# Performance work log

Measured on AMD Instinct MI355X. Metric: run time of the kernel, lower is better.

The kernel has to match this reference:

```python
import jax, jax.numpy as jnp
import numpy as np
import math

B, S, D, H, W = 4, 8192, 1024, 16, 512  # batch, seq, d_model, heads, attention_window
HD = D // H


def setup_inputs() -> dict:
    key = jax.random.key(0)
    ks = jax.random.split(key, 5)
    scale = 0.02
    return {
        "x": jax.random.normal(ks[0], (B, S, D), dtype=jnp.float32),
        "wq": jax.random.normal(ks[1], (D, D), dtype=jnp.float32) * scale,
        "bq": jnp.zeros((D,), dtype=jnp.float32),
        "wk": jax.random.normal(ks[2], (D, D), dtype=jnp.float32) * scale,
        "bk": jnp.zeros((D,), dtype=jnp.float32),
        "wv": jax.random.normal(ks[3], (D, D), dtype=jnp.float32) * scale,
        "bv": jnp.zeros((D,), dtype=jnp.float32),
        "wo": jax.random.normal(ks[4], (D, D), dtype=jnp.float32) * scale,
        "bo": jnp.zeros((D,), dtype=jnp.float32),
    }


def reference(x, wq, bq, wk, bk, wv, bv, wo, bo):
    # torch Linear: y = x @ W.T + b
    q = (x @ wq.T + bq).reshape(B, S, H, HD)
    k = (x @ wk.T + bk).reshape(B, S, H, HD)
    v = (x @ wv.T + bv).reshape(B, S, H, HD)

    nb = S // W  # number of query blocks
    qb = q.reshape(B, nb, W, H, HD)

    # pad keys/values by W at the front so every block sees a 2W key window
    kp = jnp.pad(k, ((0, 0), (W, 0), (0, 0), (0, 0)))
    vp = jnp.pad(v, ((0, 0), (W, 0), (0, 0), (0, 0)))
    # padded key indices for block n: [n*W, n*W + 2W) <-> original [n*W - W, n*W + W)
    idx = jnp.arange(nb)[:, None] * W + jnp.arange(2 * W)[None, :]  # [nb, 2W]
    kb = kp[:, idx]  # [B, nb, 2W, H, HD]
    vb = vp[:, idx]  # [B, nb, 2W, H, HD]

    scores = jnp.einsum('bnqhd,bnkhd->bnhqk', qb, kb) / math.sqrt(HD)
    valid = (idx >= W)  # padded (out-of-range) keys only occur for block 0
    scores = jnp.where(valid[None, :, None, None, :], scores, -jnp.inf)
    attn = jax.nn.softmax(scores, axis=-1)  # softmax over the block's key window

    out = jnp.einsum('bnhqk,bnkhd->bnqhd', attn, vb).reshape(B, S, D)
    return out @ wo.T + bo
```

## Files before the change

### kernel.cpp

```cpp
#include <hip/hip_runtime.h>
#include <hip/hip_bf16.h>
#include <cstdint>

typedef __bf16 bf16;
typedef __attribute__((ext_vector_type(8))) __bf16 bf16x8;
typedef __attribute__((ext_vector_type(4))) __bf16 bf16x4;
typedef __attribute__((ext_vector_type(4))) float f32x4;
typedef __attribute__((ext_vector_type(16))) float f32x16;
typedef __attribute__((ext_vector_type(4))) unsigned int u32x4;

#define B_ 4
#define S_ 8192
#define D_ 1024
#define H_ 16
#define HD_ 64
#define W_ 512
#define M_ (B_*S_)

#define EXP2F(x) __builtin_amdgcn_exp2f(x)
#define MFMA16(a,b,c) __builtin_amdgcn_mfma_f32_16x16x32_bf16(a,b,c,0,0,0)
#define MFMA32(a,b,c) __builtin_amdgcn_mfma_f32_32x32x16_bf16(a,b,c,0,0,0)

__device__ __forceinline__ void async16(const void* g, void* l) {
  __builtin_amdgcn_global_load_lds(
      (const __attribute__((address_space(1))) unsigned int*)g,
      (__attribute__((address_space(3))) unsigned int*)l, 16, 0, 0);
}

__global__ void cast_f32_bf16(const float* __restrict__ in, bf16* __restrict__ out, int n4) {
  int i = blockIdx.x * blockDim.x + threadIdx.x;
  int stride = gridDim.x * blockDim.x;
  for (; i < n4; i += stride) {
    f32x4 v = ((const f32x4*)in)[i];
    bf16x4 o = { (bf16)v[0], (bf16)v[1], (bf16)v[2], (bf16)v[3] };
    ((bf16x4*)out)[i] = o;
  }
}

template<int MODE>
__global__ void __launch_bounds__(256, 2) gemm_bt(
    const bf16* __restrict__ A, const bf16* __restrict__ Bw,
    const float* __restrict__ bias, void* __restrict__ outp, float scale)
{
  constexpr int K = D_, N = D_;
  __shared__ bf16 As[2][128*32];
  __shared__ bf16 Bs[2][128*32];
  int bid = blockIdx.x;
  int nid = (bid & 7) * 256 + (bid >> 3);
  int bm = nid >> 3, bn = nid & 7;
  const int tid = threadIdx.x, lane = tid & 63;
  const int w = tid >> 6, wr = w >> 1, wc = w & 1;
  f32x4 acc[4][4] = {};
  const int r0 = tid >> 2;
  const int kbyte = (tid & 3) * 16;
  const char* Ab = (const char*)(A + (size_t)bm * 128 * K);
  const char* Bb = (const char*)(Bw + (size_t)bn * 128 * K);

  auto stage = [&](int kt, int buf) {
    const size_t cb = (size_t)kt * 2 + kbyte;
    async16(Ab + (size_t)r0      * (K*2) + cb, (char*)&As[buf][0] + tid*16);
    async16(Ab + (size_t)(r0+64) * (K*2) + cb, (char*)&As[buf][0] + 4096 + tid*16);
    async16(Bb + (size_t)r0      * (K*2) + cb, (char*)&Bs[buf][0] + tid*16);
    async16(Bb + (size_t)(r0+64) * (K*2) + cb, (char*)&Bs[buf][0] + 4096 + tid*16);
  };

  stage(0, 0);
  for (int i = 0; i < 32; ++i) {
    int cur = i & 1;
    if (i < 31) {
      stage((i + 1) * 32, cur ^ 1);
      asm volatile("s_waitcnt vmcnt(4)" ::: "memory");
    } else {
      asm volatile("s_waitcnt vmcnt(0)" ::: "memory");
    }
    asm volatile("s_barrier" ::: "memory");
    bf16x8 a[4], b[4];
#pragma unroll
    for (int mi = 0; mi < 4; ++mi)
      a[mi] = *(const bf16x8*)(&As[cur][0] + (wr*64 + mi*16 + (lane & 15))*32 + ((lane >> 4)*8));
#pragma unroll
    for (int ni = 0; ni < 4; ++ni)
      b[ni] = *(const bf16x8*)(&Bs[cur][0] + (wc*64 + ni*16 + (lane & 15))*32 + ((lane >> 4)*8));
#pragma unroll
    for (int mi = 0; mi < 4; ++mi)
#pragma unroll
      for (int ni = 0; ni < 4; ++ni)
        acc[mi][ni] = MFMA16(a[mi], b[ni], acc[mi][ni]);
    asm volatile("s_barrier" ::: "memory");
  }
  int row0 = bm*128 + wr*64, col0 = bn*128 + wc*64;
  int rsub = (lane >> 4) * 4;
#pragma unroll
  for (int ni = 0; ni < 4; ++ni) {
    int col = col0 + ni*16 + (lane & 15);
    float bz = bias[col];
#pragma unroll
    for (int mi = 0; mi < 4; ++mi) {
#pragma unroll
      for (int r = 0; r < 4; ++r) {
        int row = row0 + mi*16 + rsub + r;
        float v = (acc[mi][ni][r] + bz) * scale;
        if (MODE == 0) {
          ((bf16*)outp)[(size_t)row * N + col] = (bf16)v;
        } else if (MODE == 1) {
          ((bf16*)outp)[((size_t)(row >> 13) * D_ + col) * S_ + (row & (S_-1))] = (bf16)v;
        } else {
          ((float*)outp)[(size_t)row * N + col] = v;
        }
      }
    }
  }
}

__global__ void __launch_bounds__(256, 3) attn_kernel(
    const bf16* __restrict__ Q, const bf16* __restrict__ Kb,
    const bf16* __restrict__ Vt, bf16* __restrict__ Ao)
{
  __shared__ char Klds[2][8192];
  __shared__ char Vlds[2][8192];
  int x = blockIdx.x;
  int qt = (x >> 3) & 3;
  int g  = (x & 7) + 8 * (x >> 5);
  int h = g & 15, n = (g >> 4) & 15, b = g >> 8;
  int tid = threadIdx.x, lane = tid & 63, w = tid >> 6;
  int hi = lane >> 5, qv = lane & 31;
  int qrow = n * W_ + qt * 128 + w * 32;

  const bf16* Qrow = Q + ((size_t)(b * S_ + qrow + qv)) * D_ + h * 64;
  bf16x8 Qf[4];
#pragma unroll
  for (int s = 0; s < 4; ++s) Qf[s] = *(const bf16x8*)(Qrow + s * 16 + hi * 8);

  const bf16* Kg = Kb + ((size_t)b * S_) * D_ + h * 64;
  const bf16* Vg = Vt + ((size_t)(b * H_ + h) * HD_) * S_;

  const int srow = tid >> 3, scol = tid & 7;
  const int sswz = (srow & 7) << 4;
  const int fswq = (qv & 7) << 4;

  f32x16 O0 = {}, O1 = {};
  float m_r = -3.0e38f, l_r = 0.f;

  const int c0 = (n == 0) ? 8 : 0;
  const int ksbase = (n - 1) * W_;

  u32x4 pk0, pk1, pv0, pv1;
  {
    int ks = ksbase + c0 * 64;
    pk0 = *(const u32x4*)(Kg + (size_t)(ks + srow)      * D_ + scol * 8);
    pk1 = *(const u32x4*)(Kg + (size_t)(ks + srow + 32) * D_ + scol * 8);
    pv0 = *(const u32x4*)(Vg + (size_t)srow        * S_ + ks + scol * 8);
    pv1 = *(const u32x4*)(Vg + (size_t)(srow + 32) * S_ + ks + scol * 8);
    *(u32x4*)(Klds[0] + srow        * 128 + ((scol * 16) ^ sswz)) = pk0;
    *(u32x4*)(Klds[0] + (srow + 32) * 128 + ((scol * 16) ^ sswz)) = pk1;
    *(u32x4*)(Vlds[0] + srow        * 128 + ((scol * 16) ^ sswz)) = pv0;
    *(u32x4*)(Vlds[0] + (srow + 32) * 128 + ((scol * 16) ^ sswz)) = pv1;
  }
  __syncthreads();
  int cur = 0;
  for (int c = c0; c < 16; ++c) {
    bool pre = (c < 15);
    if (pre) {
      int ks2 = ksbase + (c + 1) * 64;
      pk0 = *(const u32x4*)(Kg + (size_t)(ks2 + srow)      * D_ + scol * 8);
      pk1 = *(const u32x4*)(Kg + (size_t)(ks2 + srow + 32) * D_ + scol * 8);
      pv0 = *(const u32x4*)(Vg + (size_t)srow        * S_ + ks2 + scol * 8);
      pv1 = *(const u32x4*)(Vg + (size_t)(srow + 32) * S_ + ks2 + scol * 8);
    }
    const char* kbuf = Klds[cur];
    const char* vbuf = Vlds[cur];
    f32x16 C0 = {}, C1 = {};
    __builtin_amdgcn_s_setprio(1);
#pragma unroll
    for (int s = 0; s < 4; ++s) {
      bf16x8 k0 = *(const bf16x8*)(kbuf + qv * 128        + ((s * 32 + hi * 16) ^ fswq));
      bf16x8 k1 = *(const bf16x8*)(kbuf + (32 + qv) * 128 + ((s * 32 + hi * 16) ^ fswq));
      C0 = MFMA32(k0, Qf[s], C0);
      C1 = MFMA32(k1, Qf[s], C1);
    }
    __builtin_amdgcn_s_setprio(0);
    float mx = C0[0];
#pragma unroll
    for (int r = 1; r < 16; ++r) mx = fmaxf(mx, C0[r]);
#pragma unroll
    for (int r = 0; r < 16; ++r) mx = fmaxf(mx, C1[r]);
    mx = fmaxf(mx, __shfl_xor(mx, 32));
    if (!__all(mx - m_r <= 8.0f)) {
      float mn = fmaxf(m_r, mx);
      float sc = EXP2F(m_r - mn);
      m_r = mn;
      l_r *= sc;
#pragma unroll
      for (int r = 0; r < 16; ++r) { O0[r] *= sc; O1[r] *= sc; }
    }
    float ls = 0.f;
    float p0[16], p1[16];
#pragma unroll
    for (int r = 0; r < 16; ++r) {
      p0[r] = EXP2F(C0[r] - m_r);
      p1[r] = EXP2F(C1[r] - m_r);
      ls += p0[r] + p1[r];
    }
    l_r += ls;
    unsigned int L0[8], L1[8];
#pragma unroll
    for (int t = 0; t < 8; ++t) {
      asm("v_cvt_pk_bf16_f32 %0, %1, %2" : "=v"(L0[t]) : "v"(p0[2*t]), "v"(p0[2*t+1]));
      asm("v_cvt_pk_bf16_f32 %0, %1, %2" : "=v"(L1[t]) : "v"(p1[2*t]), "v"(p1[2*t+1]));
    }
    asm volatile("v_permlane32_swap_b32 %0, %1" : "+v"(L0[0]), "+v"(L0[2]));
    asm volatile("v_permlane32_swap_b32 %0, %1" : "+v"(L0[1]), "+v"(L0[3]));
    asm volatile("v_permlane32_swap_b32 %0, %1" : "+v"(L0[4]), "+v"(L0[6]));
    asm volatile("v_permlane32_swap_b32 %0, %1" : "+v"(L0[5]), "+v"(L0[7]));
    asm volatile("v_permlane32_swap_b32 %0, %1" : "+v"(L1[0]), "+v"(L1[2]));
    asm volatile("v_permlane32_swap_b32 %0, %1" : "+v"(L1[1]), "+v"(L1[3]));
    asm volatile("v_permlane32_swap_b32 %0, %1" : "+v"(L1[4]), "+v"(L1[6]));
    asm volatile("v_permlane32_swap_b32 %0, %1" : "+v"(L1[5]), "+v"(L1[7]));
    u32x4 F[2][2];
    F[0][0] = u32x4{L0[0], L0[1], L0[2], L0[3]};
    F[0][1] = u32x4{L0[4], L0[5], L0[6], L0[7]};
    F[1][0] = u32x4{L1[0], L1[1], L1[2], L1[3]};
    F[1][1] = u32x4{L1[4], L1[5], L1[6], L1[7]};
    __builtin_amdgcn_s_setprio(1);
#pragma unroll
    for (int T = 0; T < 2; ++T)
#pragma unroll
      for (int s = 0; s < 2; ++s) {
        bf16x8 pf = *(bf16x8*)&F[T][s];
        int kbyteoff = T * 64 + s * 32 + hi * 16;
        bf16x8 v0 = *(const bf16x8*)(vbuf + qv * 128        + (kbyteoff ^ fswq));
        bf16x8 v1 = *(const bf16x8*)(vbuf + (32 + qv) * 128 + (kbyteoff ^ fswq));
        O0 = MFMA32(v0, pf, O0);
        O1 = MFMA32(v1, pf, O1);
      }
    __builtin_amdgcn_s_setprio(0);
    if (pre) {
      int nb = cur ^ 1;
      *(u32x4*)(Klds[nb] + srow        * 128 + ((scol * 16) ^ sswz)) = pk0;
      *(u32x4*)(Klds[nb] + (srow + 32) * 128 + ((scol * 16) ^ sswz)) = pk1;
      *(u32x4*)(Vlds[nb] + srow        * 128 + ((scol * 16) ^ sswz)) = pv0;
      *(u32x4*)(Vlds[nb] + (srow + 32) * 128 + ((scol * 16) ^ sswz)) = pv1;
    }
    __syncthreads();
    cur ^= 1;
  }
  float lt = l_r + __shfl_xor(l_r, 32);
  float inv = 1.0f / lt;
  size_t obase = ((size_t)(b * S_ + qrow + qv)) * D_ + h * 64;
#pragma unroll
  for (int ot = 0; ot < 2; ++ot) {
#pragma unroll
    for (int rq = 0; rq < 4; ++rq) {
      int hd = ot * 32 + 8 * rq + 4 * hi;
      bf16x4 ov;
#pragma unroll
      for (int j = 0; j < 4; ++j) {
        float val = (ot == 0 ? O0[rq*4 + j] : O1[rq*4 + j]) * inv;
        ov[j] = (bf16)val;
      }
      *(bf16x4*)(Ao + obase + hd) = ov;
    }
  }
}

extern "C" void kernel_launch(void* const* d_in, const int* in_sizes, int n_in,
                              void* d_out, int out_size, void* d_ws, size_t ws_size,
                              hipStream_t stream) {
  const float* x  = (const float*)d_in[0];
  const float* wq = (const float*)d_in[1];
  const float* bq = (const float*)d_in[2];
  const float* wk = (const float*)d_in[3];
  const float* bk = (const float*)d_in[4];
  const float* wv = (const float*)d_in[5];
  const float* bv = (const float*)d_in[6];
  const float* wo = (const float*)d_in[7];
  const float* bo = (const float*)d_in[8];
  float* out = (float*)d_out;

  char* ws = (char*)d_ws;
  const size_t sz = (size_t)M_ * D_ * 2;
  bf16* xb  = (bf16*)(ws + 0*sz);
  bf16* qb  = (bf16*)(ws + 1*sz);
  bf16* kb  = (bf16*)(ws + 2*sz);
  bf16* vt  = (bf16*)(ws + 3*sz);
  bf16* ao  = (bf16*)(ws + 4*sz);
  bf16* wqb = (bf16*)(ws + 5*sz);
  bf16* wkb = wqb + (size_t)D_*D_;
  bf16* wvb = wkb + (size_t)D_*D_;
  bf16* wob = wvb + (size_t)D_*D_;

  cast_f32_bf16<<<2048, 256, 0, stream>>>(x,  xb,  M_*D_/4);
  cast_f32_bf16<<<512,  256, 0, stream>>>(wq, wqb, D_*D_/4);
  cast_f32_bf16<<<512,  256, 0, stream>>>(wk, wkb, D_*D_/4);
  cast_f32_bf16<<<512,  256, 0, stream>>>(wv, wvb, D_*D_/4);
  cast_f32_bf16<<<512,  256, 0, stream>>>(wo, wob, D_*D_/4);

  gemm_bt<0><<<2048, 256, 0, stream>>>(xb, wqb, bq, qb, 0.125f * 1.44269504f);
  gemm_bt<0><<<2048, 256, 0, stream>>>(xb, wkb, bk, kb, 1.0f);
  gemm_bt<1><<<2048, 256, 0, stream>>>(xb, wvb, bv, vt, 1.0f);

  attn_kernel<<<4096, 256, 0, stream>>>(qb, kb, vt, ao);

  gemm_bt<2><<<2048, 256, 0, stream>>>(ao, wob, bo, out, 1.0f);
}
```

Before: 575.5 us.

## Triple-buffer attention K/V with async global-to-LDS loads and fuse cast kernels

The attention kernel moves from register-staged double buffering to a three-stage ring filled by direct global-to-LDS async loads. The swizzle is applied on the global source side, and waits use explicit vmcnt plus s_barrier. This frees the VGPRs that held prefetched tiles and lets loads run two chunks ahead. The five cast launches are merged into one kernel, and the max reduction is interleaved across both score tiles. LDS per block grows from 32KB to 48KB, which may limit occupancy at 3 blocks per CU, and correctness now depends on the hand-written waitcnt accounting.

```diff
diff --git a/kernel.cpp b/kernel.cpp
--- a/kernel.cpp
+++ b/kernel.cpp
@@ -27,14 +27,28 @@
       (__attribute__((address_space(3))) unsigned int*)l, 16, 0, 0);
 }
 
-__global__ void cast_f32_bf16(const float* __restrict__ in, bf16* __restrict__ out, int n4) {
-  int i = blockIdx.x * blockDim.x + threadIdx.x;
-  int stride = gridDim.x * blockDim.x;
-  for (; i < n4; i += stride) {
+__device__ __forceinline__ void cast_region(const float* __restrict__ in,
+                                            bf16* __restrict__ out, int n4,
+                                            int i0, int stride) {
+  for (int i = i0; i < n4; i += stride) {
     f32x4 v = ((const f32x4*)in)[i];
     bf16x4 o = { (bf16)v[0], (bf16)v[1], (bf16)v[2], (bf16)v[3] };
     ((bf16x4*)out)[i] = o;
   }
+}
+
+__global__ void cast_all(const float* __restrict__ x,  bf16* __restrict__ xb,
+                         const float* __restrict__ wq, bf16* __restrict__ wqb,
+                         const float* __restrict__ wk, bf16* __restrict__ wkb,
+                         const float* __restrict__ wv, bf16* __restrict__ wvb,
+                         const float* __restrict__ wo, bf16* __restrict__ wob) {
+  int i0 = blockIdx.x * blockDim.x + threadIdx.x;
+  int stride = gridDim.x * blockDim.x;
+  cast_region(x,  xb,  M_*D_/4, i0, stride);
+  cast_region(wq, wqb, D_*D_/4, i0, stride);
+  cast_region(wk, wkb, D_*D_/4, i0, stride);
+  cast_region(wv, wvb, D_*D_/4, i0, stride);
+  cast_region(wo, wob, D_*D_/4, i0, stride);
 }
 
 template<int MODE>
@@ -116,8 +130,8 @@
     const bf16* __restrict__ Q, const bf16* __restrict__ Kb,
     const bf16* __restrict__ Vt, bf16* __restrict__ Ao)
 {
-  __shared__ char Klds[2][8192];
-  __shared__ char Vlds[2][8192];
+  __shared__ char Klds[3][8192];
+  __shared__ char Vlds[3][8192];
   int x = blockIdx.x;
   int qt = (x >> 3) & 3;
   int g  = (x & 7) + 8 * (x >> 5);
@@ -134,8 +148,8 @@
   const bf16* Kg = Kb + ((size_t)b * S_) * D_ + h * 64;
   const bf16* Vg = Vt + ((size_t)(b * H_ + h) * HD_) * S_;
 
-  const int srow = tid >> 3, scol = tid & 7;
-  const int sswz = (srow & 7) << 4;
+  const int srow = tid >> 3;
+  const int sseg = (tid & 7) ^ (srow & 7);
   const int fswq = (qv & 7) << 4;
 
   f32x16 O0 = {}, O1 = {};
@@ -144,31 +158,27 @@
   const int c0 = (n == 0) ? 8 : 0;
   const int ksbase = (n - 1) * W_;
 
-  u32x4 pk0, pk1, pv0, pv1;
-  {
-    int ks = ksbase + c0 * 64;
-    pk0 = *(const u32x4*)(Kg + (size_t)(ks + srow)      * D_ + scol * 8);
-    pk1 = *(const u32x4*)(Kg + (size_t)(ks + srow + 32) * D_ + scol * 8);
-    pv0 = *(const u32x4*)(Vg + (size_t)srow        * S_ + ks + scol * 8);
-    pv1 = *(const u32x4*)(Vg + (size_t)(srow + 32) * S_ + ks + scol * 8);
-    *(u32x4*)(Klds[0] + srow        * 128 + ((scol * 16) ^ sswz)) = pk0;
-    *(u32x4*)(Klds[0] + (srow + 32) * 128 + ((scol * 16) ^ sswz)) = pk1;
-    *(u32x4*)(Vlds[0] + srow        * 128 + ((scol * 16) ^ sswz)) = pv0;
-    *(u32x4*)(Vlds[0] + (srow + 32) * 128 + ((scol * 16) ^ sswz)) = pv1;
-  }
-  __syncthreads();
-  int cur = 0;
+  auto stage = [&](int c) {
+    int ks = ksbase + c * 64;
+    int so = (c % 3) * 8192;
+    const bf16* kr = Kg + (size_t)(ks + srow) * D_ + sseg * 8;
+    async16(kr,            &Klds[0][0] + so + tid * 16);
+    async16(kr + 32 * D_,  &Klds[0][0] + so + 4096 + tid * 16);
+    const bf16* vr = Vg + (size_t)srow * S_ + ks + sseg * 8;
+    async16(vr,            &Vlds[0][0] + so + tid * 16);
+    async16(vr + (size_t)32 * S_, &Vlds[0][0] + so + 4096 + tid * 16);
+  };
+
+  stage(c0);
+  stage(c0 + 1);
+  asm volatile("s_waitcnt vmcnt(4)" ::: "memory");
+  asm volatile("s_barrier" ::: "memory");
+
   for (int c = c0; c < 16; ++c) {
-    bool pre = (c < 15);
-    if (pre) {
-      int ks2 = ksbase + (c + 1) * 64;
-      pk0 = *(const u32x4*)(Kg + (size_t)(ks2 + srow)      * D_ + scol * 8);
-      pk1 = *(const u32x4*)(Kg + (size_t)(ks2 + srow + 32) * D_ + scol * 8);
-      pv0 = *(const u32x4*)(Vg + (size_t)srow        * S_ + ks2 + scol * 8);
-      pv1 = *(const u32x4*)(Vg + (size_t)(srow + 32) * S_ + ks2 + scol * 8);
-    }
-    const char* kbuf = Klds[cur];
-    const char* vbuf = Vlds[cur];
+    bool pre = (c + 2 < 16);
+    if (pre) stage(c + 2);
+    const char* kbuf = &Klds[0][0] + (c % 3) * 8192;
+    const char* vbuf = &Vlds[0][0] + (c % 3) * 8192;
     f32x16 C0 = {}, C1 = {};
     __builtin_amdgcn_s_setprio(1);
 #pragma unroll
@@ -179,11 +189,9 @@
       C1 = MFMA32(k1, Qf[s], C1);
     }
     __builtin_amdgcn_s_setprio(0);
-    float mx = C0[0];
-#pragma unroll
-    for (int r = 1; r < 16; ++r) mx = fmaxf(mx, C0[r]);
-#pragma unroll
-    for (int r = 0; r < 16; ++r) mx = fmaxf(mx, C1[r]);
+    float mx = fmaxf(C0[0], C1[0]);
+#pragma unroll
+    for (int r = 1; r < 16; ++r) mx = fmaxf(fmaxf(mx, C0[r]), C1[r]);
     mx = fmaxf(mx, __shfl_xor(mx, 32));
     if (!__all(mx - m_r <= 8.0f)) {
       float mn = fmaxf(m_r, mx);
@@ -235,14 +243,11 @@
       }
     __builtin_amdgcn_s_setprio(0);
     if (pre) {
-      int nb = cur ^ 1;
-      *(u32x4*)(Klds[nb] + srow        * 128 + ((scol * 16) ^ sswz)) = pk0;
-      *(u32x4*)(Klds[nb] + (srow + 32) * 128 + ((scol * 16) ^ sswz)) = pk1;
-      *(u32x4*)(Vlds[nb] + srow        * 128 + ((scol * 16) ^ sswz)) = pv0;
-      *(u32x4*)(Vlds[nb] + (srow + 32) * 128 + ((scol * 16) ^ sswz)) = pv1;
-    }
-    __syncthreads();
-    cur ^= 1;
+      asm volatile("s_waitcnt vmcnt(4)" ::: "memory");
+    } else {
+      asm volatile("s_waitcnt vmcnt(0)" ::: "memory");
+    }
+    asm volatile("s_barrier" ::: "memory");
   }
   float lt = l_r + __shfl_xor(l_r, 32);
   float inv = 1.0f / lt;
@@ -289,11 +294,7 @@
   bf16* wvb = wkb + (size_t)D_*D_;
   bf16* wob = wvb + (size_t)D_*D_;
 
-  cast_f32_bf16<<<2048, 256, 0, stream>>>(x,  xb,  M_*D_/4);
-  cast_f32_bf16<<<512,  256, 0, stream>>>(wq, wqb, D_*D_/4);
-  cast_f32_bf16<<<512,  256, 0, stream>>>(wk, wkb, D_*D_/4);
-  cast_f32_bf16<<<512,  256, 0, stream>>>(wv, wvb, D_*D_/4);
-  cast_f32_bf16<<<512,  256, 0, stream>>>(wo, wob, D_*D_/4);
+  cast_all<<<2048, 256, 0, stream>>>(x, xb, wq, wqb, wk, wkb, wv, wvb, wo, wob);
 
   gemm_bt<0><<<2048, 256, 0, stream>>>(xb, wqb, bq, qb, 0.125f * 1.44269504f);
   gemm_bt<0><<<2048, 256, 0, stream>>>(xb, wkb, bk, kb, 1.0f);
```

After: 563.2 us. 1.02x faster.
